# Kernel tuning notes

Hardware: AMD Instinct MI355X
Metric: run time of the kernel (lower is better)

The kernel has to match this reference:

```python
import jax, jax.numpy as jnp
import numpy as np

EPS = 1e-5
K = 5

def _bn(x, g, b):
    # BatchNorm1d in training mode: biased batch statistics
    mu = jnp.mean(x, axis=0)
    var = jnp.mean((x - mu) ** 2, axis=0)
    return (x - mu) * jax.lax.rsqrt(var + EPS) * g + b

def setup_inputs():
    key = jax.random.key(0)
    ks = jax.random.split(key, 16)
    N, M, D, F = 16384, 8192, 512, 2048
    s = 0.02
    return dict(
        src=jax.random.normal(ks[0], (N, D), jnp.float32),
        anchor_2=jax.random.normal(ks[1], (M, D), jnp.float32),
        W_dim=jax.random.normal(ks[2], (D, D), jnp.float32) * s,
        b_dim=jnp.zeros((D,), jnp.float32),
        W_fus=jax.random.normal(ks[3], (2 * D, D), jnp.float32) * s,
        b_fus=jnp.zeros((D,), jnp.float32),
        W_e1=jax.random.normal(ks[4], (D, F), jnp.float32) * s,
        b_e1=jnp.zeros((F,), jnp.float32),
        W_e2=jax.random.normal(ks[5], (F, D), jnp.float32) * s,
        b_e2=jnp.zeros((D,), jnp.float32),
        g1=jnp.ones((D,), jnp.float32), bt1=jnp.zeros((D,), jnp.float32),
        g2=jnp.ones((D,), jnp.float32), bt2=jnp.zeros((D,), jnp.float32),
        W_d=jax.random.normal(ks[6], (D, D), jnp.float32) * s,
        b_d=jnp.zeros((D,), jnp.float32),
        g_d=jnp.ones((D,), jnp.float32), bt_d=jnp.zeros((D,), jnp.float32),
    )

def reference(src, anchor_2, W_dim, b_dim, W_fus, b_fus, W_e1, b_e1, W_e2, b_e2,
              g1, bt1, g2, bt2, W_d, b_d, g_d, bt_d):
    # kNN in Euclidean metric (sklearn NearestNeighbors): squared distances suffice
    # d2[n,m] = ||src_n||^2 - 2 src_n . a_m + ||a_m||^2   -> [N, M]
    d2 = (jnp.sum(src * src, axis=1, keepdims=True)
          - 2.0 * (src @ anchor_2.T)
          + jnp.sum(anchor_2 * anchor_2, axis=1)[None, :])
    _, idx = jax.lax.top_k(-d2, K)                      # [N, K] nearest anchors
    neigh = jnp.mean(anchor_2[idx], axis=1)             # gather + mean -> [N, D]
    a_map = neigh @ W_dim + b_dim                       # linear_dim
    comb = jnp.concatenate([src, a_map], axis=1) @ W_fus + b_fus
    comb = _bn(comb, g1, bt1)                           # norm1
    # encoder MLP (dropout is identity in eval)
    t = jnp.tanh(comb @ W_e1 + b_e1) @ W_e2 + b_e2
    comb = _bn(comb + t, g2, bt2)                       # residual + norm2
    out = jnp.tanh(_bn(comb @ W_d + b_d, g_d, bt_d))    # decoder
    return out
```

## Files before the change

kernel.cpp:

```cpp
#include <hip/hip_runtime.h>
#include <math.h>

#define N_ROWS 16384
#define M_ANCH 8192
#define DDIM   512
#define FDIM   2048
#define KNN    5
#define BN_EPS 1e-5f
#define CHUNK  8192
#define SEED   1024
#define KSPLIT 1536
#define CAND_MAX 256

typedef _Float16 f16;
typedef _Float16 f16x8 __attribute__((ext_vector_type(8)));
typedef _Float16 f16x4 __attribute__((ext_vector_type(4)));
typedef float f32x4 __attribute__((ext_vector_type(4)));

__device__ __forceinline__ void async_copy16(const void* g, void* l) {
    __builtin_amdgcn_global_load_lds(
        (const __attribute__((address_space(1))) void*)g,
        (__attribute__((address_space(3))) void*)l, 16, 0, 0);
}

__device__ __forceinline__ bool kless(float k1, int i1, float k2, int i2) {
    return (k1 < k2) || (k1 == k2 && i1 < i2);
}

__device__ __forceinline__ void insert5(float (&bk)[KNN], int (&bi)[KNN], float key, int id) {
    if (!kless(key, id, bk[4], bi[4])) return;
    bool c3 = kless(key, id, bk[3], bi[3]);
    bool c2 = kless(key, id, bk[2], bi[2]);
    bool c1 = kless(key, id, bk[1], bi[1]);
    bool c0 = kless(key, id, bk[0], bi[0]);
    bk[4] = c3 ? bk[3] : key;                  bi[4] = c3 ? bi[3] : id;
    bk[3] = c3 ? (c2 ? bk[2] : key) : bk[3];   bi[3] = c3 ? (c2 ? bi[2] : id) : bi[3];
    bk[2] = c2 ? (c1 ? bk[1] : key) : bk[2];   bi[2] = c2 ? (c1 ? bi[1] : id) : bi[2];
    bk[1] = c1 ? (c0 ? bk[0] : key) : bk[1];   bi[1] = c1 ? (c0 ? bi[0] : id) : bi[1];
    bk[0] = c0 ? key : bk[0];                  bi[0] = c0 ? id : bi[0];
}

__global__ void zero_kernel(float* p, int n) {
    int i = blockIdx.x * blockDim.x + threadIdx.x;
    if (i < n) p[i] = 0.f;
}

template<int MODE>
__global__ __launch_bounds__(256) void split_kernel(const float* __restrict__ X,
                                                    f16* __restrict__ Y, int nrows) {
    int i4 = blockIdx.x * 256 + threadIdx.x;
    int row = i4 >> 7;
    int kc = (i4 & 127) * 4;
    if (row >= nrows) return;
    float4 v = ((const float4*)X)[i4];
    f16x4 h, lo;
    h.x = (f16)v.x; h.y = (f16)v.y; h.z = (f16)v.z; h.w = (f16)v.w;
    lo.x = (f16)(v.x - (float)h.x); lo.y = (f16)(v.y - (float)h.y);
    lo.z = (f16)(v.z - (float)h.z); lo.w = (f16)(v.w - (float)h.w);
    f16* base = Y + (size_t)row * KSPLIT + kc;
    if (MODE == 0) {
        *(f16x4*)(base) = h; *(f16x4*)(base + 512) = lo; *(f16x4*)(base + 1024) = h;
    } else {
        *(f16x4*)(base) = h; *(f16x4*)(base + 512) = h;  *(f16x4*)(base + 1024) = lo;
    }
}

__global__ __launch_bounds__(256) void anchor_norm_kernel(const float* __restrict__ a,
                                                          float* __restrict__ norm_a) {
    int wave = threadIdx.x >> 6, lane = threadIdx.x & 63;
    int row = blockIdx.x * 4 + wave;
    const float4* ar = (const float4*)(a + (size_t)row * DDIM);
    float4 v1 = ar[lane * 2];
    float4 v2 = ar[lane * 2 + 1];
    float s = v1.x*v1.x + v1.y*v1.y + v1.z*v1.z + v1.w*v1.w
            + v2.x*v2.x + v2.y*v2.y + v2.z*v2.z + v2.w*v2.w;
    for (int off = 32; off; off >>= 1) s += __shfl_xor(s, off, 64);
    if (lane == 0) norm_a[row] = s;
}

template<int K>
__global__ __launch_bounds__(256) void gemm_f16_key(
    const f16* __restrict__ A, const f16* __restrict__ B,
    const float* __restrict__ norm, float* __restrict__ C, int Ncols)
{
    __shared__ f16 As[128 * 32];
    __shared__ f16 Bs[128 * 32];
    const int t = threadIdx.x;
    const int w = t >> 6, l = t & 63;
    const int m0 = blockIdx.y * 128, n0 = blockIdx.x * 128;
    const int wm = (w & 1) * 64, wn = (w >> 1) * 64;

    f32x4 acc[4][4];
    #pragma unroll
    for (int i = 0; i < 4; ++i)
        #pragma unroll
        for (int j = 0; j < 4; ++j) acc[i][j] = (f32x4){0.f, 0.f, 0.f, 0.f};

    const int srow = l >> 2;
    const int gq = ((l & 3) - (srow >> 1)) & 3;
    const int skoff = gq * 8;
    const int sqf = (((l >> 4) + (((l & 15) >> 1) & 3)) & 3) * 8;

    for (int k0 = 0; k0 < K; k0 += 32) {
        __syncthreads();
        #pragma unroll
        for (int s = 0; s < 2; ++s) {
            int grp = w * 2 + s;
            int row = grp * 16 + srow;
            async_copy16(A + (size_t)(m0 + row) * K + k0 + skoff, As + grp * 512 + l * 8);
            async_copy16(B + (size_t)(n0 + row) * K + k0 + skoff, Bs + grp * 512 + l * 8);
        }
        __syncthreads();
        f16x8 af[4], bf[4];
        #pragma unroll
        for (int i = 0; i < 4; ++i)
            af[i] = *(const f16x8*)(As + (wm + i * 16 + (l & 15)) * 32 + sqf);
        #pragma unroll
        for (int j = 0; j < 4; ++j)
            bf[j] = *(const f16x8*)(Bs + (wn + j * 16 + (l & 15)) * 32 + sqf);
        #pragma unroll
        for (int i = 0; i < 4; ++i)
            #pragma unroll
            for (int j = 0; j < 4; ++j)
                acc[i][j] = __builtin_amdgcn_mfma_f32_16x16x32_f16(af[i], bf[j], acc[i][j], 0, 0, 0);
    }
    float nj[4];
    #pragma unroll
    for (int j = 0; j < 4; ++j) nj[j] = norm[n0 + wn + j * 16 + (l & 15)];
    #pragma unroll
    for (int i = 0; i < 4; ++i)
        #pragma unroll
        for (int j = 0; j < 4; ++j)
            #pragma unroll
            for (int r = 0; r < 4; ++r) {
                int m = m0 + wm + i * 16 + (l >> 4) * 4 + r;
                int n = n0 + wn + j * 16 + (l & 15);
                C[(size_t)m * Ncols + n] = nj[j] - 2.f * acc[i][j][r];
            }
}

template<int K>
__global__ __launch_bounds__(256) void gemm_collect(
    const f16* __restrict__ A, const f16* __restrict__ B,
    const float* __restrict__ norm, const float* __restrict__ thr,
    int* __restrict__ cnt, float* __restrict__ cand_k, int* __restrict__ cand_i,
    int idofs)
{
    __shared__ f16 As[128 * 32];
    __shared__ f16 Bs[128 * 32];
    const int t = threadIdx.x;
    const int w = t >> 6, l = t & 63;
    const int m0 = blockIdx.y * 128, n0 = blockIdx.x * 128;
    const int wm = (w & 1) * 64, wn = (w >> 1) * 64;

    f32x4 acc[4][4];
    #pragma unroll
    for (int i = 0; i < 4; ++i)
        #pragma unroll
        for (int j = 0; j < 4; ++j) acc[i][j] = (f32x4){0.f, 0.f, 0.f, 0.f};

    const int srow = l >> 2;
    const int gq = ((l & 3) - (srow >> 1)) & 3;
    const int skoff = gq * 8;
    const int sqf = (((l >> 4) + (((l & 15) >> 1) & 3)) & 3) * 8;

    for (int k0 = 0; k0 < K; k0 += 32) {
        __syncthreads();
        #pragma unroll
        for (int s = 0; s < 2; ++s) {
            int grp = w * 2 + s;
            int row = grp * 16 + srow;
            async_copy16(A + (size_t)(m0 + row) * K + k0 + skoff, As + grp * 512 + l * 8);
            async_copy16(B + (size_t)(n0 + row) * K + k0 + skoff, Bs + grp * 512 + l * 8);
        }
        __syncthreads();
        f16x8 af[4], bf[4];
        #pragma unroll
        for (int i = 0; i < 4; ++i)
            af[i] = *(const f16x8*)(As + (wm + i * 16 + (l & 15)) * 32 + sqf);
        #pragma unroll
        for (int j = 0; j < 4; ++j)
            bf[j] = *(const f16x8*)(Bs + (wn + j * 16 + (l & 15)) * 32 + sqf);
        #pragma unroll
        for (int i = 0; i < 4; ++i)
            #pragma unroll
            for (int j = 0; j < 4; ++j)
                acc[i][j] = __builtin_amdgcn_mfma_f32_16x16x32_f16(af[i], bf[j], acc[i][j], 0, 0, 0);
    }
    float thr4[4][4];
    #pragma unroll
    for (int i = 0; i < 4; ++i) {
        float4 tv = *(const float4*)&thr[m0 + wm + i * 16 + (l >> 4) * 4];
        thr4[i][0] = tv.x; thr4[i][1] = tv.y; thr4[i][2] = tv.z; thr4[i][3] = tv.w;
    }
    float nj[4];
    #pragma unroll
    for (int j = 0; j < 4; ++j) nj[j] = norm[n0 + wn + j * 16 + (l & 15)];
    #pragma unroll
    for (int i = 0; i < 4; ++i)
        #pragma unroll
        for (int j = 0; j < 4; ++j)
            #pragma unroll
            for (int r = 0; r < 4; ++r) {
                float key = nj[j] - 2.f * acc[i][j][r];
                if (key < thr4[i][r]) {
                    int row = m0 + wm + i * 16 + (l >> 4) * 4 + r;
                    int pos = atomicAdd(&cnt[row], 1);
                    if (pos < CAND_MAX) {
                        cand_k[(size_t)row * CAND_MAX + pos] = key;
                        cand_i[(size_t)row * CAND_MAX + pos] =
                            idofs + n0 + wn + j * 16 + (l & 15);
                    }
                }
            }
}

__global__ __launch_bounds__(256) void topk_scan_kernel(
    const float* __restrict__ g, float* __restrict__ bk_state,
    int* __restrict__ bi_state, float* __restrict__ thrbuf)
{
    int row = blockIdx.x * 4 + (threadIdx.x >> 6);
    int lane = threadIdx.x & 63;
    const float* grow = g + (size_t)row * SEED;
    float4 v0 = *(const float4*)(grow + lane * 4);
    float4 v1 = *(const float4*)(grow + 256 + lane * 4);
    float4 v2 = *(const float4*)(grow + 512 + lane * 4);
    float4 v3 = *(const float4*)(grow + 768 + lane * 4);
    float bk[KNN]; int bi[KNN];
    #pragma unroll
    for (int q = 0; q < KNN; ++q) { bk[q] = 3.0e38f; bi[q] = 0x7fffffff; }
    int c = lane * 4;
    insert5(bk, bi, v0.x, c);       insert5(bk, bi, v0.y, c + 1);
    insert5(bk, bi, v0.z, c + 2);   insert5(bk, bi, v0.w, c + 3);
    insert5(bk, bi, v1.x, c + 256); insert5(bk, bi, v1.y, c + 257);
    insert5(bk, bi, v1.z, c + 258); insert5(bk, bi, v1.w, c + 259);
    insert5(bk, bi, v2.x, c + 512); insert5(bk, bi, v2.y, c + 513);
    insert5(bk, bi, v2.z, c + 514); insert5(bk, bi, v2.w, c + 515);
    insert5(bk, bi, v3.x, c + 768); insert5(bk, bi, v3.y, c + 769);
    insert5(bk, bi, v3.z, c + 770); insert5(bk, bi, v3.w, c + 771);
    for (int off = 32; off >= 1; off >>= 1) {
        float ok[KNN]; int oi[KNN];
        #pragma unroll
        for (int q = 0; q < KNN; ++q) {
            ok[q] = __shfl_xor(bk[q], off, 64);
            oi[q] = __shfl_xor(bi[q], off, 64);
        }
        #pragma unroll
        for (int q = 0; q < KNN; ++q) insert5(bk, bi, ok[q], oi[q]);
    }
    if (lane == 0) {
        #pragma unroll
        for (int q = 0; q < KNN; ++q) {
            bk_state[row * KNN + q] = bk[q];
            bi_state[row * KNN + q] = bi[q];
        }
        thrbuf[row] = bk[4];
    }
}

__global__ __launch_bounds__(256) void cand_merge_kernel(
    const int* __restrict__ cnt, const float* __restrict__ cand_k,
    const int* __restrict__ cand_i, float* __restrict__ bk_state,
    int* __restrict__ bi_state)
{
    int row = blockIdx.x * 256 + threadIdx.x;
    if (row >= N_ROWS) return;
    float bk[KNN]; int bi[KNN];
    #pragma unroll
    for (int q = 0; q < KNN; ++q) {
        bk[q] = bk_state[row * KNN + q];
        bi[q] = bi_state[row * KNN + q];
    }
    int c = cnt[row]; if (c > CAND_MAX) c = CAND_MAX;
    const float* ck = cand_k + (size_t)row * CAND_MAX;
    const int*   ci = cand_i + (size_t)row * CAND_MAX;
    for (int p = 0; p < c; ++p) insert5(bk, bi, ck[p], ci[p]);
    #pragma unroll
    for (int q = 0; q < KNN; ++q) bi_state[row * KNN + q] = bi[q];
}

__global__ __launch_bounds__(256) void gather_mean_kernel(
    const float* __restrict__ anchor, const int* __restrict__ bi_state,
    float* __restrict__ neigh)
{
    int row = blockIdx.x * 4 + (threadIdx.x >> 6);
    int lane = threadIdx.x & 63;
    const int* bi = bi_state + row * KNN;
    int i0 = bi[0], i1 = bi[1], i2 = bi[2], i3 = bi[3], i4 = bi[4];
    const float4* a0 = (const float4*)(anchor + (size_t)i0 * DDIM);
    const float4* a1 = (const float4*)(anchor + (size_t)i1 * DDIM);
    const float4* a2 = (const float4*)(anchor + (size_t)i2 * DDIM);
    const float4* a3 = (const float4*)(anchor + (size_t)i3 * DDIM);
    const float4* a4 = (const float4*)(anchor + (size_t)i4 * DDIM);
    float4* np = (float4*)(neigh + (size_t)row * DDIM);
    #pragma unroll
    for (int p = 0; p < 2; ++p) {
        int c4 = lane + 64 * p;
        float4 v0 = a0[c4], v1 = a1[c4], v2 = a2[c4], v3 = a3[c4], v4 = a4[c4];
        float4 o;
        o.x = (v0.x + v1.x + v2.x + v3.x + v4.x) * 0.2f;
        o.y = (v0.y + v1.y + v2.y + v3.y + v4.y) * 0.2f;
        o.z = (v0.z + v1.z + v2.z + v3.z + v4.z) * 0.2f;
        o.w = (v0.w + v1.w + v2.w + v3.w + v4.w) * 0.2f;
        np[c4] = o;
    }
}

template<int ADDC0, int TANH, int K>
__global__ __launch_bounds__(256) void gemm_split_nt(
    const float* __restrict__ A, const f16* __restrict__ Bw,
    const float* __restrict__ bias, const float* __restrict__ C0,
    float* __restrict__ C, int Ncols)
{
    __shared__ f16 Ah[128 * 32];
    __shared__ f16 Al[128 * 32];
    __shared__ f16 Bh[128 * 32];
    __shared__ f16 Bl[128 * 32];
    const int t = threadIdx.x;
    const int w = t >> 6, l = t & 63;
    const int m0 = blockIdx.y * 128, n0 = blockIdx.x * 128;
    const int wm = (w & 1) * 64, wn = (w >> 1) * 64;
    const int K2 = 2 * K;

    f32x4 acc[4][4];
    #pragma unroll
    for (int i = 0; i < 4; ++i)
        #pragma unroll
        for (int j = 0; j < 4; ++j) acc[i][j] = (f32x4){0.f, 0.f, 0.f, 0.f};

    const int ar = t >> 1;
    const int ac = (t & 1) * 16;
    const int arq = (ar >> 1) & 3;
    const int s0 = (((t & 1) * 2 + 0 + arq) & 3) * 8;
    const int s1 = (((t & 1) * 2 + 1 + arq) & 3) * 8;
    const int srow = l >> 2;
    const int gq = ((l & 3) - (srow >> 1)) & 3;
    const int skoff = gq * 8;
    const int sqf = (((l >> 4) + (((l & 15) >> 1) & 3)) & 3) * 8;

    for (int k0 = 0; k0 < K; k0 += 32) {
        __syncthreads();
        #pragma unroll
        for (int s = 0; s < 2; ++s) {
            int grp = w * 2 + s;
            int row = grp * 16 + srow;
            const f16* bp = Bw + (size_t)(n0 + row) * K2 + k0 + skoff;
            async_copy16(bp, Bh + grp * 512 + l * 8);
            async_copy16(bp + K, Bl + grp * 512 + l * 8);
        }
        {
            const float* ap = A + (size_t)(m0 + ar) * K + k0 + ac;
            float xs[16];
            *(float4*)&xs[0]  = *(const float4*)ap;
            *(float4*)&xs[4]  = *(const float4*)(ap + 4);
            *(float4*)&xs[8]  = *(const float4*)(ap + 8);
            *(float4*)&xs[12] = *(const float4*)(ap + 12);
            f16x8 h0, h1, lo0, lo1;
            #pragma unroll
            for (int e = 0; e < 8; ++e) {
                f16 hh = (f16)xs[e];
                h0[e] = hh; lo0[e] = (f16)(xs[e] - (float)hh);
                f16 hh2 = (f16)xs[8 + e];
                h1[e] = hh2; lo1[e] = (f16)(xs[8 + e] - (float)hh2);
            }
            *(f16x8*)&Ah[ar * 32 + s0] = h0;  *(f16x8*)&Ah[ar * 32 + s1] = h1;
            *(f16x8*)&Al[ar * 32 + s0] = lo0; *(f16x8*)&Al[ar * 32 + s1] = lo1;
        }
        __syncthreads();
        f16x8 afh[4], afl[4], bfh[4], bfl[4];
        #pragma unroll
        for (int i = 0; i < 4; ++i) {
            int base = (wm + i * 16 + (l & 15)) * 32 + sqf;
            afh[i] = *(const f16x8*)(Ah + base);
            afl[i] = *(const f16x8*)(Al + base);
        }
        #pragma unroll
        for (int j = 0; j < 4; ++j) {
            int base = (wn + j * 16 + (l & 15)) * 32 + sqf;
            bfh[j] = *(const f16x8*)(Bh + base);
            bfl[j] = *(const f16x8*)(Bl + base);
        }
        #pragma unroll
        for (int i = 0; i < 4; ++i)
            #pragma unroll
            for (int j = 0; j < 4; ++j) {
                acc[i][j] = __builtin_amdgcn_mfma_f32_16x16x32_f16(afh[i], bfh[j], acc[i][j], 0, 0, 0);
                acc[i][j] = __builtin_amdgcn_mfma_f32_16x16x32_f16(afl[i], bfh[j], acc[i][j], 0, 0, 0);
                acc[i][j] = __builtin_amdgcn_mfma_f32_16x16x32_f16(afh[i], bfl[j], acc[i][j], 0, 0, 0);
            }
    }
    float bv[4];
    #pragma unroll
    for (int j = 0; j < 4; ++j)
        bv[j] = bias ? bias[n0 + wn + j * 16 + (l & 15)] : 0.f;
    #pragma unroll
    for (int i = 0; i < 4; ++i)
        #pragma unroll
        for (int j = 0; j < 4; ++j)
            #pragma unroll
            for (int r = 0; r < 4; ++r) {
                int m = m0 + wm + i * 16 + (l >> 4) * 4 + r;
                int n = n0 + wn + j * 16 + (l & 15);
                float v = acc[i][j][r] + bv[j];
                if (ADDC0) v += C0[(size_t)m * Ncols + n];
                if (TANH)  v = tanhf(v);
                C[(size_t)m * Ncols + n] = v;
            }
}

__global__ __launch_bounds__(256) void wsplit_kernel(const float* __restrict__ W,
                                                     f16* __restrict__ Wt,
                                                     int K, int N)
{
    __shared__ float tile[64][65];
    const int t = threadIdx.x;
    const int kb = blockIdx.y * 64, nb = blockIdx.x * 64;
    #pragma unroll
    for (int i = 0; i < 4; ++i) {
        int r = (t >> 4) + i * 16;
        int c = (t & 15) * 4;
        *(float4*)&tile[r][c] = *(const float4*)&W[(size_t)(kb + r) * N + nb + c];
    }
    __syncthreads();
    const int r2 = t >> 2;
    const int kc = (t & 3) * 16;
    f16x8 h0, h1, lo0, lo1;
    #pragma unroll
    for (int e = 0; e < 8; ++e) {
        float x = tile[kc + e][r2];
        f16 hh = (f16)x; h0[e] = hh; lo0[e] = (f16)(x - (float)hh);
        float y = tile[kc + 8 + e][r2];
        f16 hh2 = (f16)y; h1[e] = hh2; lo1[e] = (f16)(y - (float)hh2);
    }
    f16* base = Wt + (size_t)(nb + r2) * 2 * K + kb + kc;
    *(f16x8*)base = h0; *(f16x8*)(base + 8) = h1;
    *(f16x8*)(base + K) = lo0; *(f16x8*)(base + K + 8) = lo1;
}

__global__ __launch_bounds__(256) void bcomb_kernel(const float* __restrict__ b_dim,
                                                    const float* __restrict__ W_fus2,
                                                    const float* __restrict__ b_fus,
                                                    float* __restrict__ b_comb)
{
    int n = blockIdx.x * 256 + threadIdx.x;
    if (n >= DDIM) return;
    float s = b_fus[n];
    for (int k = 0; k < DDIM; ++k) s += b_dim[k] * W_fus2[(size_t)k * DDIM + n];
    b_comb[n] = s;
}

template<int ACT>
__global__ __launch_bounds__(256) void gemm_kernel(
    const float* __restrict__ A, int K1,
    const float* __restrict__ A2, int K2,
    const float* __restrict__ B, const float* __restrict__ bias,
    float* __restrict__ C, int Ncols)
{
    __shared__ float As[16][132];
    __shared__ float Bs[16][128];
    const int t = threadIdx.x;
    const int n0 = blockIdx.x * 128;
    const int m0 = blockIdx.y * 128;
    const int ty = t >> 4, tx = t & 15;
    const int K = K1 + K2;

    float acc[8][8];
    #pragma unroll
    for (int i = 0; i < 8; ++i)
        #pragma unroll
        for (int j = 0; j < 8; ++j) acc[i][j] = 0.f;

    const int ar = t >> 1;
    const int akc = (t & 1) * 8;
    const int bkr = t >> 4;
    const int bc = (t & 15) * 8;

    for (int k0 = 0; k0 < K; k0 += 16) {
        int kk = k0 + akc;
        float4 v0, v1;
        if (kk < K1) {
            const float* p = A + (size_t)(m0 + ar) * K1 + kk;
            v0 = *(const float4*)p; v1 = *(const float4*)(p + 4);
        } else {
            const float* p = A2 + (size_t)(m0 + ar) * K2 + (kk - K1);
            v0 = *(const float4*)p; v1 = *(const float4*)(p + 4);
        }
        const float* bp = B + (size_t)(k0 + bkr) * Ncols + n0 + bc;
        float4 w0 = *(const float4*)bp, w1 = *(const float4*)(bp + 4);
        __syncthreads();
        As[akc+0][ar] = v0.x; As[akc+1][ar] = v0.y; As[akc+2][ar] = v0.z; As[akc+3][ar] = v0.w;
        As[akc+4][ar] = v1.x; As[akc+5][ar] = v1.y; As[akc+6][ar] = v1.z; As[akc+7][ar] = v1.w;
        *(float4*)&Bs[bkr][bc] = w0; *(float4*)&Bs[bkr][bc + 4] = w1;
        __syncthreads();
        #pragma unroll
        for (int k = 0; k < 16; ++k) {
            float a[8], b[8];
            *(float4*)&a[0] = *(const float4*)&As[k][ty * 8];
            *(float4*)&a[4] = *(const float4*)&As[k][ty * 8 + 4];
            *(float4*)&b[0] = *(const float4*)&Bs[k][tx * 4];
            *(float4*)&b[4] = *(const float4*)&Bs[k][64 + tx * 4];
            #pragma unroll
            for (int i = 0; i < 8; ++i)
                #pragma unroll
                for (int j = 0; j < 8; ++j) acc[i][j] += a[i] * b[j];
        }
    }
    float4 bv0 = *(const float4*)(bias + n0 + tx * 4);
    float4 bv1 = *(const float4*)(bias + n0 + 64 + tx * 4);
    #pragma unroll
    for (int i = 0; i < 8; ++i) {
        int row = m0 + ty * 8 + i;
        float4 o0, o1;
        o0.x = acc[i][0] + bv0.x; o0.y = acc[i][1] + bv0.y;
        o0.z = acc[i][2] + bv0.z; o0.w = acc[i][3] + bv0.w;
        o1.x = acc[i][4] + bv1.x; o1.y = acc[i][5] + bv1.y;
        o1.z = acc[i][6] + bv1.z; o1.w = acc[i][7] + bv1.w;
        if (ACT == 1) {
            o0.x = tanhf(o0.x); o0.y = tanhf(o0.y); o0.z = tanhf(o0.z); o0.w = tanhf(o0.w);
            o1.x = tanhf(o1.x); o1.y = tanhf(o1.y); o1.z = tanhf(o1.z); o1.w = tanhf(o1.w);
        }
        *(float4*)(C + (size_t)row * Ncols + n0 + tx * 4) = o0;
        *(float4*)(C + (size_t)row * Ncols + n0 + 64 + tx * 4) = o1;
    }
}

__global__ __launch_bounds__(256) void bn_stats_kernel(const float* __restrict__ X,
                                                       float* __restrict__ sums)
{
    __shared__ float red[8][64];
    int lane = threadIdx.x & 63;
    int rl = threadIdx.x >> 6;
    int c = blockIdx.x * 64 + lane;
    int chunk = N_ROWS / gridDim.y;
    int rbeg = blockIdx.y * chunk;
    float s = 0.f, s2 = 0.f;
    for (int r = rbeg + rl; r < rbeg + chunk; r += 4) {
        float v = X[(size_t)r * DDIM + c];
        s += v; s2 += v * v;
    }
    red[rl][lane] = s; red[4 + rl][lane] = s2;
    __syncthreads();
    if (threadIdx.x < 64) {
        float ts = red[0][lane] + red[1][lane] + red[2][lane] + red[3][lane];
        float t2 = red[4][lane] + red[5][lane] + red[6][lane] + red[7][lane];
        atomicAdd(&sums[c], ts);
        atomicAdd(&sums[DDIM + c], t2);
    }
}

template<int TANH>
__global__ __launch_bounds__(256) void bn_apply_kernel(
    const float* __restrict__ X, float* __restrict__ Y,
    const float* __restrict__ sums, const float* __restrict__ g,
    const float* __restrict__ b, float invN)
{
    size_t i = (size_t)blockIdx.x * 256 + threadIdx.x;
    int cg = (int)(i % (DDIM / 4));
    int c = cg * 4;
    float4 x = ((const float4*)X)[i];
    float4 sm = *(const float4*)(sums + c);
    float4 sq = *(const float4*)(sums + DDIM + c);
    float4 gv = *(const float4*)(g + c);
    float4 bv = *(const float4*)(b + c);
    float m, var, rs;
    m = sm.x * invN; var = sq.x * invN - m * m; rs = rsqrtf(var + BN_EPS);
    x.x = (x.x - m) * rs * gv.x + bv.x;
    m = sm.y * invN; var = sq.y * invN - m * m; rs = rsqrtf(var + BN_EPS);
    x.y = (x.y - m) * rs * gv.y + bv.y;
    m = sm.z * invN; var = sq.z * invN - m * m; rs = rsqrtf(var + BN_EPS);
    x.z = (x.z - m) * rs * gv.z + bv.z;
    m = sm.w * invN; var = sq.w * invN - m * m; rs = rsqrtf(var + BN_EPS);
    x.w = (x.w - m) * rs * gv.w + bv.w;
    if (TANH) { x.x = tanhf(x.x); x.y = tanhf(x.y); x.z = tanhf(x.z); x.w = tanhf(x.w); }
    ((float4*)Y)[i] = x;
}

extern "C" void kernel_launch(void* const* d_in, const int* in_sizes, int n_in,
                              void* d_out, int out_size, void* d_ws, size_t ws_size,
                              hipStream_t stream)
{
    const float* src   = (const float*)d_in[0];
    const float* anc   = (const float*)d_in[1];
    const float* W_dim = (const float*)d_in[2];
    const float* b_dim = (const float*)d_in[3];
    const float* W_fus = (const float*)d_in[4];
    const float* b_fus = (const float*)d_in[5];
    const float* W_e1  = (const float*)d_in[6];
    const float* b_e1  = (const float*)d_in[7];
    const float* W_e2  = (const float*)d_in[8];
    const float* b_e2  = (const float*)d_in[9];
    const float* g1    = (const float*)d_in[10];
    const float* bt1   = (const float*)d_in[11];
    const float* g2    = (const float*)d_in[12];
    const float* bt2   = (const float*)d_in[13];
    const float* W_d   = (const float*)d_in[14];
    const float* b_d   = (const float*)d_in[15];
    const float* g_d   = (const float*)d_in[16];
    const float* bt_d  = (const float*)d_in[17];
    float* out = (float*)d_out;

    float* ws = (float*)d_ws;
    float* score  = ws;
    float* bufA   = ws + 16777216;
    f16*   src2   = (f16*)(ws + 25165824);
    f16*   anc2   = (f16*)(ws + 37748736);
    f16*   wbase  = (f16*)(ws + 25165824);
    f16*   Wt_fus1  = wbase;
    f16*   Wt_comb2 = wbase + 524288;
    f16*   Wt_e1    = wbase + 1048576;
    f16*   Wt_e2    = wbase + 3145728;
    f16*   Wt_d     = wbase + 5242880;
    float* W_comb2  = ws + 44040192;
    float* norm_a   = ws + 44302336;
    float* sums1    = ws + 44310528;
    float* sums2    = sums1 + 1024;
    float* sums3    = sums2 + 1024;
    float* zeros512 = ws + 44313600;
    float* b_comb   = ws + 44314112;
    float* bk_state = ws + 44314624;
    int*   bi_state = (int*)(ws + 44396544);
    float* thrbuf   = ws + 44478464;
    int*   cnt      = (int*)(ws + 44494848);
    float* cand_k   = ws + 44511232;
    int*   cand_i   = (int*)(ws + 48705536);

    const float invN = 1.0f / (float)N_ROWS;
    float* hbuf = score;

    zero_kernel<<<dim3(14), 256, 0, stream>>>(sums1, 3584);
    zero_kernel<<<dim3(64), 256, 0, stream>>>((float*)cnt, 16384);
    split_kernel<0><<<dim3(N_ROWS * DDIM / 1024), 256, 0, stream>>>(src, src2, N_ROWS);
    split_kernel<1><<<dim3(M_ANCH * DDIM / 1024), 256, 0, stream>>>(anc, anc2, M_ANCH);
    anchor_norm_kernel<<<dim3(M_ANCH / 4), 256, 0, stream>>>(anc, norm_a);

    gemm_f16_key<KSPLIT><<<dim3(SEED / 128, N_ROWS / 128), 256, 0, stream>>>(
        src2, anc2, norm_a, score, SEED);
    topk_scan_kernel<<<dim3(N_ROWS / 4), 256, 0, stream>>>(
        score, bk_state, bi_state, thrbuf);
    gemm_collect<KSPLIT><<<dim3((M_ANCH - SEED) / 128, N_ROWS / 128), 256, 0, stream>>>(
        src2, anc2 + (size_t)SEED * KSPLIT, norm_a + SEED, thrbuf,
        cnt, cand_k, cand_i, SEED);
    cand_merge_kernel<<<dim3(64), 256, 0, stream>>>(cnt, cand_k, cand_i,
                                                    bk_state, bi_state);
    gather_mean_kernel<<<dim3(N_ROWS / 4), 256, 0, stream>>>(anc, bi_state, bufA);

    wsplit_kernel<<<dim3(DDIM / 64, DDIM / 64), 256, 0, stream>>>(W_fus, Wt_fus1, DDIM, DDIM);
    wsplit_kernel<<<dim3(FDIM / 64, DDIM / 64), 256, 0, stream>>>(W_e1, Wt_e1, DDIM, FDIM);
    wsplit_kernel<<<dim3(DDIM / 64, FDIM / 64), 256, 0, stream>>>(W_e2, Wt_e2, FDIM, DDIM);
    wsplit_kernel<<<dim3(DDIM / 64, DDIM / 64), 256, 0, stream>>>(W_d, Wt_d, DDIM, DDIM);
    gemm_kernel<0><<<dim3(4, 4), 256, 0, stream>>>(
        W_dim, DDIM, nullptr, 0, W_fus + DDIM * DDIM, zeros512, W_comb2, DDIM);
    bcomb_kernel<<<dim3(2), 256, 0, stream>>>(b_dim, W_fus + DDIM * DDIM, b_fus, b_comb);
    wsplit_kernel<<<dim3(DDIM / 64, DDIM / 64), 256, 0, stream>>>(W_comb2, Wt_comb2, DDIM, DDIM);

    gemm_split_nt<0, 0, DDIM><<<dim3(DDIM / 128, N_ROWS / 128), 256, 0, stream>>>(
        src, Wt_fus1, b_comb, nullptr, out, DDIM);
    gemm_split_nt<1, 0, DDIM><<<dim3(DDIM / 128, N_ROWS / 128), 256, 0, stream>>>(
        bufA, Wt_comb2, nullptr, out, out, DDIM);
    bn_stats_kernel<<<dim3(DDIM / 64, 16), 256, 0, stream>>>(out, sums1);
    bn_apply_kernel<0><<<dim3(8192), 256, 0, stream>>>(out, out, sums1, g1, bt1, invN);

    for (int r0 = 0; r0 < N_ROWS; r0 += CHUNK) {
        gemm_split_nt<0, 1, DDIM><<<dim3(FDIM / 128, CHUNK / 128), 256, 0, stream>>>(
            out + (size_t)r0 * DDIM, Wt_e1, b_e1, nullptr, hbuf, FDIM);
        gemm_split_nt<1, 0, FDIM><<<dim3(DDIM / 128, CHUNK / 128), 256, 0, stream>>>(
            hbuf, Wt_e2, b_e2, out + (size_t)r0 * DDIM, bufA + (size_t)r0 * DDIM,
            DDIM);
    }
    bn_stats_kernel<<<dim3(DDIM / 64, 16), 256, 0, stream>>>(bufA, sums2);
    bn_apply_kernel<0><<<dim3(8192), 256, 0, stream>>>(bufA, bufA, sums2, g2, bt2, invN);

    gemm_split_nt<0, 0, DDIM><<<dim3(DDIM / 128, N_ROWS / 128), 256, 0, stream>>>(
        bufA, Wt_d, b_d, nullptr, out, DDIM);
    bn_stats_kernel<<<dim3(DDIM / 64, 16), 256, 0, stream>>>(out, sums3);
    bn_apply_kernel<1><<<dim3(8192), 256, 0, stream>>>(out, out, sums3, g_d, bt_d, invN);
}
```

Baseline: 1.731 ms.

## Use single-f16 kNN screening with margin, then rescore candidates in fp32

The kNN distance GEMMs drop the three-term f16 split (K=1536) and use a single f16 cast (K=512), cutting screening GEMM work by about three times. To keep results exact, candidates within a fixed margin of the approximate 5th-best distance are collected from both the seed and remaining blocks. A new rescore kernel then recomputes exact fp32 distances for each row's candidates and selects the top 5. This adds a gather-heavy rescoring pass. It risks missing true neighbours if f16 error exceeds the margin, or overflowing CAND_MAX if the margin admits too many candidates.

Result: faster. 1.607 ms (-7.2%).

```diff
diff --git a/kernel.cpp b/kernel.cpp
--- a/kernel.cpp
+++ b/kernel.cpp
@@ -9,8 +9,8 @@
 #define BN_EPS 1e-5f
 #define CHUNK  8192
 #define SEED   1024
-#define KSPLIT 1536
 #define CAND_MAX 256
+#define MARGIN 4.0f
 
 typedef _Float16 f16;
 typedef _Float16 f16x8 __attribute__((ext_vector_type(8)));
@@ -45,24 +45,14 @@
     if (i < n) p[i] = 0.f;
 }
 
-template<int MODE>
-__global__ __launch_bounds__(256) void split_kernel(const float* __restrict__ X,
-                                                    f16* __restrict__ Y, int nrows) {
+__global__ __launch_bounds__(256) void cast_f16_kernel(const float* __restrict__ X,
+                                                       f16* __restrict__ Y, int n4) {
     int i4 = blockIdx.x * 256 + threadIdx.x;
-    int row = i4 >> 7;
-    int kc = (i4 & 127) * 4;
-    if (row >= nrows) return;
+    if (i4 >= n4) return;
     float4 v = ((const float4*)X)[i4];
-    f16x4 h, lo;
+    f16x4 h;
     h.x = (f16)v.x; h.y = (f16)v.y; h.z = (f16)v.z; h.w = (f16)v.w;
-    lo.x = (f16)(v.x - (float)h.x); lo.y = (f16)(v.y - (float)h.y);
-    lo.z = (f16)(v.z - (float)h.z); lo.w = (f16)(v.w - (float)h.w);
-    f16* base = Y + (size_t)row * KSPLIT + kc;
-    if (MODE == 0) {
-        *(f16x4*)(base) = h; *(f16x4*)(base + 512) = lo; *(f16x4*)(base + 1024) = h;
-    } else {
-        *(f16x4*)(base) = h; *(f16x4*)(base + 512) = h;  *(f16x4*)(base + 1024) = lo;
-    }
+    ((f16x4*)Y)[i4] = h;
 }
 
 __global__ __launch_bounds__(256) void anchor_norm_kernel(const float* __restrict__ a,
@@ -143,8 +133,7 @@
 __global__ __launch_bounds__(256) void gemm_collect(
     const f16* __restrict__ A, const f16* __restrict__ B,
     const float* __restrict__ norm, const float* __restrict__ thr,
-    int* __restrict__ cnt, float* __restrict__ cand_k, int* __restrict__ cand_i,
-    int idofs)
+    int* __restrict__ cnt, int* __restrict__ cand_i, int idofs)
 {
     __shared__ f16 As[128 * 32];
     __shared__ f16 Bs[128 * 32];
@@ -206,18 +195,16 @@
                 if (key < thr4[i][r]) {
                     int row = m0 + wm + i * 16 + (l >> 4) * 4 + r;
                     int pos = atomicAdd(&cnt[row], 1);
-                    if (pos < CAND_MAX) {
-                        cand_k[(size_t)row * CAND_MAX + pos] = key;
+                    if (pos < CAND_MAX)
                         cand_i[(size_t)row * CAND_MAX + pos] =
                             idofs + n0 + wn + j * 16 + (l & 15);
-                    }
                 }
             }
 }
 
 __global__ __launch_bounds__(256) void topk_scan_kernel(
-    const float* __restrict__ g, float* __restrict__ bk_state,
-    int* __restrict__ bi_state, float* __restrict__ thrbuf)
+    const float* __restrict__ g, float* __restrict__ thrbuf,
+    int* __restrict__ cnt, int* __restrict__ cand_i)
 {
     int row = blockIdx.x * 4 + (threadIdx.x >> 6);
     int lane = threadIdx.x & 63;
@@ -248,35 +235,47 @@
         #pragma unroll
         for (int q = 0; q < KNN; ++q) insert5(bk, bi, ok[q], oi[q]);
     }
+    float thr = bk[4] + MARGIN;
+    if (lane == 0) thrbuf[row] = thr;
+    int* rci = cand_i + (size_t)row * CAND_MAX;
+    #define PUSH(v, id) if ((v) < thr) { int pos = atomicAdd(&cnt[row], 1); \
+                                         if (pos < CAND_MAX) rci[pos] = (id); }
+    PUSH(v0.x, c)       PUSH(v0.y, c + 1)   PUSH(v0.z, c + 2)   PUSH(v0.w, c + 3)
+    PUSH(v1.x, c + 256) PUSH(v1.y, c + 257) PUSH(v1.z, c + 258) PUSH(v1.w, c + 259)
+    PUSH(v2.x, c + 512) PUSH(v2.y, c + 513) PUSH(v2.z, c + 514) PUSH(v2.w, c + 515)
+    PUSH(v3.x, c + 768) PUSH(v3.y, c + 769) PUSH(v3.z, c + 770) PUSH(v3.w, c + 771)
+    #undef PUSH
+}
+
+__global__ __launch_bounds__(256) void rescore_kernel(
+    const float* __restrict__ src, const float* __restrict__ anchor,
+    const float* __restrict__ norm_a, const int* __restrict__ cnt,
+    const int* __restrict__ cand_i, int* __restrict__ bi_state)
+{
+    int row = blockIdx.x * 4 + (threadIdx.x >> 6);
+    int lane = threadIdx.x & 63;
+    const float4* sp = (const float4*)(src + (size_t)row * DDIM);
+    float4 s0 = sp[lane * 2], s1 = sp[lane * 2 + 1];
+    float bk[KNN]; int bi[KNN];
+    #pragma unroll
+    for (int q = 0; q < KNN; ++q) { bk[q] = 3.0e38f; bi[q] = 0x7fffffff; }
+    int c = cnt[row]; if (c > CAND_MAX) c = CAND_MAX;
+    const int* ci = cand_i + (size_t)row * CAND_MAX;
+    for (int p = 0; p < c; ++p) {
+        int id = ci[p];
+        const float4* ap = (const float4*)(anchor + (size_t)id * DDIM);
+        float4 a0 = ap[lane * 2], a1 = ap[lane * 2 + 1];
+        float d = s0.x*a0.x + s0.y*a0.y + s0.z*a0.z + s0.w*a0.w
+                + s1.x*a1.x + s1.y*a1.y + s1.z*a1.z + s1.w*a1.w;
+        #pragma unroll
+        for (int off = 32; off; off >>= 1) d += __shfl_xor(d, off, 64);
+        float key = norm_a[id] - 2.f * d;
+        insert5(bk, bi, key, id);
+    }
     if (lane == 0) {
         #pragma unroll
-        for (int q = 0; q < KNN; ++q) {
-            bk_state[row * KNN + q] = bk[q];
-            bi_state[row * KNN + q] = bi[q];
-        }
-        thrbuf[row] = bk[4];
-    }
-}
-
-__global__ __launch_bounds__(256) void cand_merge_kernel(
-    const int* __restrict__ cnt, const float* __restrict__ cand_k,
-    const int* __restrict__ cand_i, float* __restrict__ bk_state,
-    int* __restrict__ bi_state)
-{
-    int row = blockIdx.x * 256 + threadIdx.x;
-    if (row >= N_ROWS) return;
-    float bk[KNN]; int bi[KNN];
-    #pragma unroll
-    for (int q = 0; q < KNN; ++q) {
-        bk[q] = bk_state[row * KNN + q];
-        bi[q] = bi_state[row * KNN + q];
-    }
-    int c = cnt[row]; if (c > CAND_MAX) c = CAND_MAX;
-    const float* ck = cand_k + (size_t)row * CAND_MAX;
-    const int*   ci = cand_i + (size_t)row * CAND_MAX;
-    for (int p = 0; p < c; ++p) insert5(bk, bi, ck[p], ci[p]);
-    #pragma unroll
-    for (int q = 0; q < KNN; ++q) bi_state[row * KNN + q] = bi[q];
+        for (int q = 0; q < KNN; ++q) bi_state[row * KNN + q] = bi[q];
+    }
 }
 
 __global__ __launch_bounds__(256) void gather_mean_kernel(
@@ -602,8 +601,8 @@
     float* ws = (float*)d_ws;
     float* score  = ws;
     float* bufA   = ws + 16777216;
-    f16*   src2   = (f16*)(ws + 25165824);
-    f16*   anc2   = (f16*)(ws + 37748736);
+    f16*   src2h  = (f16*)(ws + 25165824);
+    f16*   anc2h  = (f16*)(ws + 37748736);
     f16*   wbase  = (f16*)(ws + 25165824);
     f16*   Wt_fus1  = wbase;
     f16*   Wt_comb2 = wbase + 524288;
@@ -617,11 +616,9 @@
     float* sums3    = sums2 + 1024;
     float* zeros512 = ws + 44313600;
     float* b_comb   = ws + 44314112;
-    float* bk_state = ws + 44314624;
     int*   bi_state = (int*)(ws + 44396544);
     float* thrbuf   = ws + 44478464;
     int*   cnt      = (int*)(ws + 44494848);
-    float* cand_k   = ws + 44511232;
     int*   cand_i   = (int*)(ws + 48705536);
 
     const float invN = 1.0f / (float)N_ROWS;
@@ -629,19 +626,21 @@
 
     zero_kernel<<<dim3(14), 256, 0, stream>>>(sums1, 3584);
     zero_kernel<<<dim3(64), 256, 0, stream>>>((float*)cnt, 16384);
-    split_kernel<0><<<dim3(N_ROWS * DDIM / 1024), 256, 0, stream>>>(src, src2, N_ROWS);
-    split_kernel<1><<<dim3(M_ANCH * DDIM / 1024), 256, 0, stream>>>(anc, anc2, M_ANCH);
+    cast_f16_kernel<<<dim3(N_ROWS * DDIM / 1024), 256, 0, stream>>>(
+        src, src2h, N_ROWS * DDIM / 4);
+    cast_f16_kernel<<<dim3(M_ANCH * DDIM / 1024), 256, 0, stream>>>(
+        anc, anc2h, M_ANCH * DDIM / 4);
     anchor_norm_kernel<<<dim3(M_ANCH / 4), 256, 0, stream>>>(anc, norm_a);
 
-    gemm_f16_key<KSPLIT><<<dim3(SEED / 128, N_ROWS / 128), 256, 0, stream>>>(
-        src2, anc2, norm_a, score, SEED);
+    gemm_f16_key<DDIM><<<dim3(SEED / 128, N_ROWS / 128), 256, 0, stream>>>(
+        src2h, anc2h, norm_a, score, SEED);
     topk_scan_kernel<<<dim3(N_ROWS / 4), 256, 0, stream>>>(
-        score, bk_state, bi_state, thrbuf);
-    gemm_collect<KSPLIT><<<dim3((M_ANCH - SEED) / 128, N_ROWS / 128), 256, 0, stream>>>(
-        src2, anc2 + (size_t)SEED * KSPLIT, norm_a + SEED, thrbuf,
-        cnt, cand_k, cand_i, SEED);
-    cand_merge_kernel<<<dim3(64), 256, 0, stream>>>(cnt, cand_k, cand_i,
-                                                    bk_state, bi_state);
+        score, thrbuf, cnt, cand_i);
+    gemm_collect<DDIM><<<dim3((M_ANCH - SEED) / 128, N_ROWS / 128), 256, 0, stream>>>(
+        src2h, anc2h + (size_t)SEED * DDIM, norm_a + SEED, thrbuf,
+        cnt, cand_i, SEED);
+    rescore_kernel<<<dim3(N_ROWS / 4), 256, 0, stream>>>(
+        src, anc, norm_a, cnt, cand_i, bi_state);
     gather_mean_kernel<<<dim3(N_ROWS / 4), 256, 0, stream>>>(anc, bi_state, bufA);
 
     wsplit_kernel<<<dim3(DDIM / 64, DDIM / 64), 256, 0, stream>>>(W_fus, Wt_fus1, DDIM, DDIM);
```
